# Kernel optimization log

Hardware: AMD Instinct MI355X
Metric: run time of the kernel (lower is better)

## Reference

```python
import jax, jax.numpy as jnp
import numpy as np

N, D, F = 4096, 4096, 16384  # tokens, d_model, d_ff


def setup_inputs() -> dict:
    key = jax.random.key(0)
    ks = jax.random.split(key, 8)
    q_in = jax.random.randint(ks[0], (N, D), -127, 128, dtype=jnp.int32)
    in_scale = jax.random.uniform(ks[1], (N,), dtype=jnp.float32) * 0.01 + 1e-4
    w1_q = jax.random.randint(ks[2], (F, D), -127, 128, dtype=jnp.int32)
    w1_scale = jax.random.uniform(ks[3], (F,), dtype=jnp.float32) * 0.01 + 1e-4
    b1 = jax.random.normal(ks[4], (F,), dtype=jnp.float32) * 0.02
    w2_q = jax.random.randint(ks[5], (D, F), -127, 128, dtype=jnp.int32)
    w2_scale = jax.random.uniform(ks[6], (D,), dtype=jnp.float32) * 0.01 + 1e-4
    b2 = jax.random.normal(ks[7], (D,), dtype=jnp.float32) * 0.02
    return {"q_in": q_in, "in_scale": in_scale, "w1_q": w1_q, "w1_scale": w1_scale,
            "b1": b1, "w2_q": w2_q, "w2_scale": w2_scale, "b2": b2}


def _dynamic_quant(x):
    # per-token abs-max dynamic quantization to int8 range
    s = jnp.max(jnp.abs(x), axis=-1, keepdims=True) / 127.0
    s = jnp.maximum(s, 1e-8)
    q = jnp.clip(jnp.round(x / s), -128.0, 127.0)
    return q, s


def reference(q_in, in_scale, w1_q, w1_scale, b1, w2_q, w2_scale, b2):
    y1 = jnp.einsum('nd,fd->nf', q_in.astype(jnp.float32), w1_q.astype(jnp.float32))
    y1 = y1 * in_scale[:, None] * w1_scale[None, :] + b1[None, :]
    # fused gelu + dynamic re-quantization epilogue
    a = jax.nn.gelu(y1, approximate=False)
    q2, s2 = _dynamic_quant(a)
    # fc2
    y2 = jnp.einsum('nf,df->nd', q2, w2_q.astype(jnp.float32))
    y2 = y2 * s2 * w2_scale[None, :] + b2[None, :]
    return y2
```

## Files before the change

kernel.cpp:

```cpp
#include <hip/hip_runtime.h>
#include <hip/hip_bf16.h>
#include <cstdint>
#include <math.h>

#define TOKENS 4096
#define DMODEL 4096
#define DFF    16384

typedef __attribute__((ext_vector_type(4))) int i32x4;
typedef __attribute__((address_space(1))) unsigned int glb_u32;
typedef __attribute__((address_space(3))) unsigned int lds_u32;

__global__ void pack_i8_kernel(const int* __restrict__ src, unsigned* __restrict__ dst, long n4) {
    long i = (long)blockIdx.x * blockDim.x + threadIdx.x;
    const long stride = (long)gridDim.x * blockDim.x;
    for (; i < n4; i += stride) {
        const int4 v = ((const int4*)src)[i];
        unsigned p = (unsigned(v.x) & 255u) | ((unsigned(v.y) & 255u) << 8) |
                     ((unsigned(v.z) & 255u) << 16) | ((unsigned(v.w) & 255u) << 24);
        dst[i] = p;
    }
}

__global__ void zero_u32_kernel(unsigned* __restrict__ p, int n) {
    int i = blockIdx.x * blockDim.x + threadIdx.x;
    if (i < n) p[i] = 0u;
}

template <int EPI>
__global__ __launch_bounds__(512)
void gemm_i8_kernel(const int8_t* __restrict__ A,
                    const int8_t* __restrict__ B,
                    const int Nout, const int K,
                    const float* __restrict__ scaleA,
                    const float* __restrict__ scaleB,
                    const float* __restrict__ bias,
                    unsigned* __restrict__ rowmax,
                    __hip_bfloat16* __restrict__ aout,
                    float* __restrict__ out)
{
    __shared__ int8_t As[2][256 * 128];
    __shared__ int8_t Bs[2][256 * 128];

    const int tid  = threadIdx.x;
    const int lane = tid & 63;
    const int w    = tid >> 6;
    const int wm   = w >> 2;
    const int wn   = w & 3;
    const int l15  = lane & 15, l4 = lane >> 4;

    const int gx  = gridDim.x;
    const int nwg = gx * gridDim.y;
    int wg = blockIdx.y * gx + blockIdx.x;
    wg = (wg & 7) * (nwg >> 3) + (wg >> 3);
    const int col0 = (wg % gx) * 256;
    const int row0 = (wg / gx) * 256;

    const int nt = K >> 7;

    const int rw = (w << 3) + (lane >> 3);
    const int g16 = ((lane & 7) ^ (lane >> 3)) << 4;

    const int rbA = (((wm << 7) + l15) << 7);
    const int rbB = (((wn << 6) + l15) << 7);
    const int c0  = (l4 ^ (l15 & 7)) << 4;

    i32x4 acc[8][4] = {};

#define STAGE_OP(P, p0q, LDSBUF, t)                                                   \
    {                                                                                 \
        const int k0_ = (t) << 7;                                                     \
        const int8_t* src_ = (P) + (size_t)((p0q) + (w << 3) + (lane >> 3)) * K +     \
                             k0_ + g16;                                               \
        int8_t* dst_ = &LDSBUF[(t) & 1][w << 10];                                     \
        _Pragma("unroll")                                                             \
        for (int u_ = 0; u_ < 4; ++u_)                                                \
            __builtin_amdgcn_global_load_lds((glb_u32*)(src_ + (size_t)(u_ * 64) * K),\
                                             (lds_u32*)(dst_ + u_ * 8192), 16, 0, 0); \
    }

    STAGE_OP(A, row0, As, 0);
    STAGE_OP(B, col0, Bs, 0);
    STAGE_OP(A, row0, As, 1);
    STAGE_OP(B, col0, Bs, 1);
    asm volatile("s_waitcnt vmcnt(8)" ::: "memory");
    __builtin_amdgcn_s_barrier();

    for (int t = 0; t < nt; ++t) {
        const int buf = t & 1;
        const int tn = (t + 2 < nt) ? (t + 2) : (nt - 1);
        i32x4 a0[8], b0[4], a1[8], b1[4];

#pragma unroll
        for (int m = 0; m < 8; ++m)
            a0[m] = *(const i32x4*)(&As[buf][rbA + m * 2048 + c0]);
#pragma unroll
        for (int n = 0; n < 4; ++n)
            b0[n] = *(const i32x4*)(&Bs[buf][rbB + n * 2048 + c0]);
        asm volatile("s_waitcnt lgkmcnt(0)" ::: "memory");
        __builtin_amdgcn_sched_barrier(0);
        __builtin_amdgcn_s_setprio(1);
#pragma unroll
        for (int m = 0; m < 4; ++m)
#pragma unroll
            for (int n = 0; n < 4; ++n)
                acc[m][n] = __builtin_amdgcn_mfma_i32_16x16x64_i8(a0[m], b0[n], acc[m][n], 0, 0, 0);
        __builtin_amdgcn_s_setprio(0);
        __builtin_amdgcn_s_barrier();

#pragma unroll
        for (int m = 0; m < 8; ++m)
            a1[m] = *(const i32x4*)(&As[buf][rbA + m * 2048 + (c0 ^ 64)]);
#pragma unroll
        for (int n = 0; n < 4; ++n)
            b1[n] = *(const i32x4*)(&Bs[buf][rbB + n * 2048 + (c0 ^ 64)]);
        __builtin_amdgcn_s_setprio(1);
#pragma unroll
        for (int m = 4; m < 8; ++m)
#pragma unroll
            for (int n = 0; n < 4; ++n)
                acc[m][n] = __builtin_amdgcn_mfma_i32_16x16x64_i8(a0[m], b0[n], acc[m][n], 0, 0, 0);
        __builtin_amdgcn_s_setprio(0);
        asm volatile("s_waitcnt lgkmcnt(0)" ::: "memory");
        __builtin_amdgcn_sched_barrier(0);
        __builtin_amdgcn_s_barrier();

        STAGE_OP(A, row0, As, tn);
        __builtin_amdgcn_s_setprio(1);
#pragma unroll
        for (int m = 0; m < 4; ++m)
#pragma unroll
            for (int n = 0; n < 4; ++n)
                acc[m][n] = __builtin_amdgcn_mfma_i32_16x16x64_i8(a1[m], b1[n], acc[m][n], 0, 0, 0);
        __builtin_amdgcn_s_setprio(0);
        __builtin_amdgcn_s_barrier();

        STAGE_OP(B, col0, Bs, tn);
        __builtin_amdgcn_s_setprio(1);
#pragma unroll
        for (int m = 4; m < 8; ++m)
#pragma unroll
            for (int n = 0; n < 4; ++n)
                acc[m][n] = __builtin_amdgcn_mfma_i32_16x16x64_i8(a1[m], b1[n], acc[m][n], 0, 0, 0);
        __builtin_amdgcn_s_setprio(0);
        asm volatile("s_waitcnt vmcnt(8)" ::: "memory");
        __builtin_amdgcn_s_barrier();
    }
#undef STAGE_OP

    if (EPI == 1) {
#pragma unroll
        for (int m = 0; m < 8; ++m) {
#pragma unroll
            for (int reg = 0; reg < 4; ++reg) {
                const int grow = row0 + (wm << 7) + m * 16 + l4 * 4 + reg;
                const float sa = scaleA[grow];
                float vmax = 0.0f;
#pragma unroll
                for (int n = 0; n < 4; ++n) {
                    const int gcol = col0 + (wn << 6) + n * 16 + l15;
                    const float y = (float)acc[m][n][reg] * sa * scaleB[gcol] + bias[gcol];
                    const float gl = 0.5f * y * (1.0f + erff(y * 0.70710678118654752f));
                    aout[(size_t)grow * DFF + gcol] = __float2bfloat16(gl);
                    vmax = fmaxf(vmax, fabsf(gl));
                }
#pragma unroll
                for (int off = 1; off < 16; off <<= 1)
                    vmax = fmaxf(vmax, __shfl_xor(vmax, off));
                if (l15 == 0) atomicMax(&rowmax[grow], __float_as_uint(vmax));
            }
        }
    } else {
#pragma unroll
        for (int m = 0; m < 8; ++m) {
#pragma unroll
            for (int reg = 0; reg < 4; ++reg) {
                const int grow = row0 + (wm << 7) + m * 16 + l4 * 4 + reg;
                const float s2 = fmaxf(__uint_as_float(rowmax[grow]) * (1.0f / 127.0f), 1e-8f);
#pragma unroll
                for (int n = 0; n < 4; ++n) {
                    const int gcol = col0 + (wn << 6) + n * 16 + l15;
                    out[(size_t)grow * Nout + gcol] =
                        (float)acc[m][n][reg] * s2 * scaleB[gcol] + bias[gcol];
                }
            }
        }
    }
}

__global__ void quant_kernel(const unsigned short* __restrict__ a,
                             const unsigned* __restrict__ rowmax,
                             int8_t* __restrict__ q2)
{
    const size_t nvec = (size_t)TOKENS * DFF / 8;
    size_t i = (size_t)blockIdx.x * blockDim.x + threadIdx.x;
    const size_t stride = (size_t)gridDim.x * blockDim.x;
    for (; i < nvec; i += stride) {
        const size_t e0 = i * 8;
        const int n = (int)(e0 >> 14);
        const float s2 = fmaxf(__uint_as_float(rowmax[n]) * (1.0f / 127.0f), 1e-8f);
        const float inv = 1.0f / s2;
        const uint4 v = *(const uint4*)(a + e0);
        const unsigned words[4] = {v.x, v.y, v.z, v.w};
        int qi[8];
#pragma unroll
        for (int j = 0; j < 4; ++j) {
            const float f0 = __uint_as_float((words[j] & 0xffffu) << 16);
            const float f1 = __uint_as_float(words[j] & 0xffff0000u);
            qi[2 * j]     = (int)fminf(fmaxf(rintf(f0 * inv), -128.0f), 127.0f);
            qi[2 * j + 1] = (int)fminf(fmaxf(rintf(f1 * inv), -128.0f), 127.0f);
        }
        const unsigned p0 = (unsigned(qi[0]) & 255u) | ((unsigned(qi[1]) & 255u) << 8) |
                            ((unsigned(qi[2]) & 255u) << 16) | ((unsigned(qi[3]) & 255u) << 24);
        const unsigned p1 = (unsigned(qi[4]) & 255u) | ((unsigned(qi[5]) & 255u) << 8) |
                            ((unsigned(qi[6]) & 255u) << 16) | ((unsigned(qi[7]) & 255u) << 24);
        ((uint2*)q2)[i] = make_uint2(p0, p1);
    }
}

extern "C" void kernel_launch(void* const* d_in, const int* in_sizes, int n_in,
                              void* d_out, int out_size, void* d_ws, size_t ws_size,
                              hipStream_t stream) {
    const int*   q_in     = (const int*)d_in[0];
    const float* in_scale = (const float*)d_in[1];
    const int*   w1_q     = (const int*)d_in[2];
    const float* w1_scale = (const float*)d_in[3];
    const float* b1       = (const float*)d_in[4];
    const int*   w2_q     = (const int*)d_in[5];
    const float* w2_scale = (const float*)d_in[6];
    const float* b2       = (const float*)d_in[7];
    float* out = (float*)d_out;

    char* ws = (char*)d_ws;
    int8_t* A1 = (int8_t*)(ws);
    int8_t* W1 = (int8_t*)(ws + (size_t)16  * 1048576);
    int8_t* W2 = (int8_t*)(ws + (size_t)80  * 1048576);
    int8_t* Q2 = (int8_t*)(ws + (size_t)144 * 1048576);
    unsigned short* ABUF = (unsigned short*)(ws + (size_t)208 * 1048576);
    unsigned* ROWMAX = (unsigned*)(ws + (size_t)336 * 1048576);

    zero_u32_kernel<<<dim3(16), dim3(256), 0, stream>>>(ROWMAX, TOKENS);
    pack_i8_kernel<<<dim3(1024), dim3(256), 0, stream>>>(q_in, (unsigned*)A1, (long)TOKENS * DMODEL / 4);
    pack_i8_kernel<<<dim3(4096), dim3(256), 0, stream>>>(w1_q, (unsigned*)W1, (long)DFF * DMODEL / 4);
    pack_i8_kernel<<<dim3(4096), dim3(256), 0, stream>>>(w2_q, (unsigned*)W2, (long)DMODEL * DFF / 4);

    gemm_i8_kernel<1><<<dim3(DFF / 256, TOKENS / 256), dim3(512), 0, stream>>>(
        A1, W1, DFF, DMODEL, in_scale, w1_scale, b1, ROWMAX,
        (__hip_bfloat16*)ABUF, nullptr);

    quant_kernel<<<dim3(4096), dim3(256), 0, stream>>>(ABUF, ROWMAX, Q2);

    gemm_i8_kernel<2><<<dim3(DMODEL / 256, TOKENS / 256), dim3(512), 0, stream>>>(
        Q2, W2, DMODEL, DFF, nullptr, w2_scale, b2, ROWMAX,
        nullptr, out);
}
```

Measured before the change: 851.8 us.

## Switch GEMM to 32x32x32 int8 MFMA with software-pipelined LDS fragment reads

Replaces the 16x16x64 int8 MFMA tiling with 32x32x32 MFMAs, so each wave holds a 4x2 grid of 16-element accumulators, and rewrites the LDS swizzle addressing to match. The K loop now prefetches fragment slices for the next tile before the current tile's last MFMA slice, with graded lgkmcnt waits, to overlap LDS reads with MFMA work. Both global loads for the tile two ahead are issued together after a single barrier. The epilogue row/column mapping and the row-max shuffle reduction are updated for the 32-wide layout. This adds register pressure and depends on the new swizzle mapping being correct.

```diff
diff --git a/kernel.cpp b/kernel.cpp
--- a/kernel.cpp
+++ b/kernel.cpp
@@ -7,7 +7,8 @@
 #define DMODEL 4096
 #define DFF    16384
 
-typedef __attribute__((ext_vector_type(4))) int i32x4;
+typedef __attribute__((ext_vector_type(4)))  int i32x4;
+typedef __attribute__((ext_vector_type(16))) int i32x16;
 typedef __attribute__((address_space(1))) unsigned int glb_u32;
 typedef __attribute__((address_space(3))) unsigned int lds_u32;
 
@@ -47,7 +48,7 @@
     const int w    = tid >> 6;
     const int wm   = w >> 2;
     const int wn   = w & 3;
-    const int l15  = lane & 15, l4 = lane >> 4;
+    const int l31  = lane & 31, l5 = lane >> 5, cx = lane & 7;
 
     const int gx  = gridDim.x;
     const int nwg = gx * gridDim.y;
@@ -58,14 +59,37 @@
 
     const int nt = K >> 7;
 
-    const int rw = (w << 3) + (lane >> 3);
     const int g16 = ((lane & 7) ^ (lane >> 3)) << 4;
 
-    const int rbA = (((wm << 7) + l15) << 7);
-    const int rbB = (((wn << 6) + l15) << 7);
-    const int c0  = (l4 ^ (l15 & 7)) << 4;
-
-    i32x4 acc[8][4] = {};
+    const int rbA = ((wm << 7) + l31) << 7;
+    const int rbB = ((wn << 6) + l31) << 7;
+#define AOFF(m, s) (rbA + (m) * 4096 + (((((s) << 1) | l5) ^ cx) << 4))
+#define BOFF(n, s) (rbB + (n) * 4096 + (((((s) << 1) | l5) ^ cx) << 4))
+
+    i32x4 fA[4][4], fB[4][2];
+    i32x16 acc[4][2] = {};
+
+#define READ_SLICE(s, bufi)                                                       \
+    {                                                                             \
+        _Pragma("unroll")                                                         \
+        for (int m_ = 0; m_ < 4; ++m_)                                            \
+            fA[s][m_] = *(const i32x4*)(&As[bufi][AOFF(m_, s)]);                  \
+        _Pragma("unroll")                                                         \
+        for (int n_ = 0; n_ < 2; ++n_)                                            \
+            fB[s][n_] = *(const i32x4*)(&Bs[bufi][BOFF(n_, s)]);                  \
+    }
+
+#define MFMA_SLICE(s)                                                             \
+    {                                                                             \
+        __builtin_amdgcn_s_setprio(1);                                            \
+        _Pragma("unroll")                                                         \
+        for (int m_ = 0; m_ < 4; ++m_)                                            \
+            _Pragma("unroll")                                                     \
+            for (int n_ = 0; n_ < 2; ++n_)                                        \
+                acc[m_][n_] = __builtin_amdgcn_mfma_i32_32x32x32_i8(              \
+                    fA[s][m_], fB[s][n_], acc[m_][n_], 0, 0, 0);                  \
+        __builtin_amdgcn_s_setprio(0);                                            \
+    }
 
 #define STAGE_OP(P, p0q, LDSBUF, t)                                                   \
     {                                                                                 \
@@ -85,101 +109,80 @@
     STAGE_OP(B, col0, Bs, 1);
     asm volatile("s_waitcnt vmcnt(8)" ::: "memory");
     __builtin_amdgcn_s_barrier();
+    READ_SLICE(0, 0);
+    READ_SLICE(1, 0);
 
     for (int t = 0; t < nt; ++t) {
         const int buf = t & 1;
-        const int tn = (t + 2 < nt) ? (t + 2) : (nt - 1);
-        i32x4 a0[8], b0[4], a1[8], b1[4];
-
-#pragma unroll
-        for (int m = 0; m < 8; ++m)
-            a0[m] = *(const i32x4*)(&As[buf][rbA + m * 2048 + c0]);
-#pragma unroll
-        for (int n = 0; n < 4; ++n)
-            b0[n] = *(const i32x4*)(&Bs[buf][rbB + n * 2048 + c0]);
+        const int tn1 = (t + 1 < nt) ? (t + 1) : (nt - 1);
+        const int tn2 = (t + 2 < nt) ? (t + 2) : (nt - 1);
+
+        READ_SLICE(2, buf);
+        asm volatile("s_waitcnt lgkmcnt(12)" ::: "memory");
+        __builtin_amdgcn_sched_barrier(0);
+        MFMA_SLICE(0);
+
+        READ_SLICE(3, buf);
+        asm volatile("s_waitcnt lgkmcnt(12)" ::: "memory");
+        __builtin_amdgcn_sched_barrier(0);
+        MFMA_SLICE(1);
+
+        asm volatile("s_waitcnt lgkmcnt(6)" ::: "memory");
+        __builtin_amdgcn_sched_barrier(0);
+        MFMA_SLICE(2);
+
         asm volatile("s_waitcnt lgkmcnt(0)" ::: "memory");
         __builtin_amdgcn_sched_barrier(0);
-        __builtin_amdgcn_s_setprio(1);
-#pragma unroll
-        for (int m = 0; m < 4; ++m)
-#pragma unroll
-            for (int n = 0; n < 4; ++n)
-                acc[m][n] = __builtin_amdgcn_mfma_i32_16x16x64_i8(a0[m], b0[n], acc[m][n], 0, 0, 0);
-        __builtin_amdgcn_s_setprio(0);
         __builtin_amdgcn_s_barrier();
 
-#pragma unroll
-        for (int m = 0; m < 8; ++m)
-            a1[m] = *(const i32x4*)(&As[buf][rbA + m * 2048 + (c0 ^ 64)]);
-#pragma unroll
-        for (int n = 0; n < 4; ++n)
-            b1[n] = *(const i32x4*)(&Bs[buf][rbB + n * 2048 + (c0 ^ 64)]);
-        __builtin_amdgcn_s_setprio(1);
-#pragma unroll
-        for (int m = 4; m < 8; ++m)
-#pragma unroll
-            for (int n = 0; n < 4; ++n)
-                acc[m][n] = __builtin_amdgcn_mfma_i32_16x16x64_i8(a0[m], b0[n], acc[m][n], 0, 0, 0);
-        __builtin_amdgcn_s_setprio(0);
-        asm volatile("s_waitcnt lgkmcnt(0)" ::: "memory");
-        __builtin_amdgcn_sched_barrier(0);
-        __builtin_amdgcn_s_barrier();
-
-        STAGE_OP(A, row0, As, tn);
-        __builtin_amdgcn_s_setprio(1);
-#pragma unroll
-        for (int m = 0; m < 4; ++m)
-#pragma unroll
-            for (int n = 0; n < 4; ++n)
-                acc[m][n] = __builtin_amdgcn_mfma_i32_16x16x64_i8(a1[m], b1[n], acc[m][n], 0, 0, 0);
-        __builtin_amdgcn_s_setprio(0);
-        __builtin_amdgcn_s_barrier();
-
-        STAGE_OP(B, col0, Bs, tn);
-        __builtin_amdgcn_s_setprio(1);
-#pragma unroll
-        for (int m = 4; m < 8; ++m)
-#pragma unroll
-            for (int n = 0; n < 4; ++n)
-                acc[m][n] = __builtin_amdgcn_mfma_i32_16x16x64_i8(a1[m], b1[n], acc[m][n], 0, 0, 0);
-        __builtin_amdgcn_s_setprio(0);
+        STAGE_OP(A, row0, As, tn2);
+        STAGE_OP(B, col0, Bs, tn2);
         asm volatile("s_waitcnt vmcnt(8)" ::: "memory");
         __builtin_amdgcn_s_barrier();
+
+        READ_SLICE(0, tn1 & 1);
+        READ_SLICE(1, tn1 & 1);
+        MFMA_SLICE(3);
     }
 #undef STAGE_OP
+#undef READ_SLICE
+#undef MFMA_SLICE
+#undef AOFF
+#undef BOFF
 
     if (EPI == 1) {
 #pragma unroll
-        for (int m = 0; m < 8; ++m) {
-#pragma unroll
-            for (int reg = 0; reg < 4; ++reg) {
-                const int grow = row0 + (wm << 7) + m * 16 + l4 * 4 + reg;
+        for (int m = 0; m < 4; ++m) {
+#pragma unroll
+            for (int reg = 0; reg < 16; ++reg) {
+                const int grow = row0 + (wm << 7) + m * 32 + (reg & 3) + 8 * (reg >> 2) + 4 * l5;
                 const float sa = scaleA[grow];
                 float vmax = 0.0f;
-#pragma unroll
-                for (int n = 0; n < 4; ++n) {
-                    const int gcol = col0 + (wn << 6) + n * 16 + l15;
+                float gl[2];
+#pragma unroll
+                for (int n = 0; n < 2; ++n) {
+                    const int gcol = col0 + (wn << 6) + n * 32 + l31;
                     const float y = (float)acc[m][n][reg] * sa * scaleB[gcol] + bias[gcol];
-                    const float gl = 0.5f * y * (1.0f + erff(y * 0.70710678118654752f));
-                    aout[(size_t)grow * DFF + gcol] = __float2bfloat16(gl);
-                    vmax = fmaxf(vmax, fabsf(gl));
+                    gl[n] = 0.5f * y * (1.0f + erff(y * 0.70710678118654752f));
+                    aout[(size_t)grow * DFF + gcol] = __float2bfloat16(gl[n]);
+                    vmax = fmaxf(vmax, fabsf(gl[n]));
                 }
 #pragma unroll
-                for (int off = 1; off < 16; off <<= 1)
+                for (int off = 1; off < 32; off <<= 1)
                     vmax = fmaxf(vmax, __shfl_xor(vmax, off));
-                if (l15 == 0) atomicMax(&rowmax[grow], __float_as_uint(vmax));
+                if (l31 == 0) atomicMax(&rowmax[grow], __float_as_uint(vmax));
             }
         }
     } else {
 #pragma unroll
-        for (int m = 0; m < 8; ++m) {
-#pragma unroll
-            for (int reg = 0; reg < 4; ++reg) {
-                const int grow = row0 + (wm << 7) + m * 16 + l4 * 4 + reg;
+        for (int m = 0; m < 4; ++m) {
+#pragma unroll
+            for (int reg = 0; reg < 16; ++reg) {
+                const int grow = row0 + (wm << 7) + m * 32 + (reg & 3) + 8 * (reg >> 2) + 4 * l5;
                 const float s2 = fmaxf(__uint_as_float(rowmax[grow]) * (1.0f / 127.0f), 1e-8f);
 #pragma unroll
-                for (int n = 0; n < 4; ++n) {
-                    const int gcol = col0 + (wn << 6) + n * 16 + l15;
+                for (int n = 0; n < 2; ++n) {
+                    const int gcol = col0 + (wn << 6) + n * 32 + l31;
                     out[(size_t)grow * Nout + gcol] =
                         (float)acc[m][n][reg] * s2 * scaleB[gcol] + bias[gcol];
                 }
```

Result: slower. 1.041 ms (+22.3%).

## Restructure int8 GEMM main loop into 1-ahead prefetch with interleaved per-unit loads

Applied to the files above, without the earlier changes.

Replaces the 2-tile-ahead prefetch with a one-tile-ahead double buffer. Global-to-LDS loads are split into per-unit issues placed between the four MFMA quarters, and the A fragments are loaded as half-sized lo/hi groups to cut register use. The aim is to spread memory traffic evenly across the compute phases and lower VGPR pressure. The cost is a shallower prefetch distance, which may expose more global-memory latency, plus extra barriers per iteration.

```diff
diff --git a/kernel.cpp b/kernel.cpp
--- a/kernel.cpp
+++ b/kernel.cpp
@@ -58,95 +58,105 @@
 
     const int nt = K >> 7;
 
-    const int rw = (w << 3) + (lane >> 3);
     const int g16 = ((lane & 7) ^ (lane >> 3)) << 4;
 
     const int rbA = (((wm << 7) + l15) << 7);
     const int rbB = (((wn << 6) + l15) << 7);
     const int c0  = (l4 ^ (l15 & 7)) << 4;
 
+    i32x4 fAlo[4], fAhi[4], fB[4];
     i32x4 acc[8][4] = {};
 
-#define STAGE_OP(P, p0q, LDSBUF, t)                                                   \
+#define STAGE_UNIT(P, p0q, LDSARR, bufi, t, u)                                        \
     {                                                                                 \
-        const int k0_ = (t) << 7;                                                     \
-        const int8_t* src_ = (P) + (size_t)((p0q) + (w << 3) + (lane >> 3)) * K +     \
-                             k0_ + g16;                                               \
-        int8_t* dst_ = &LDSBUF[(t) & 1][w << 10];                                     \
+        const int8_t* src_ = (P) + (size_t)((p0q) + (u) * 64 + (w << 3) +             \
+                             (lane >> 3)) * K + ((t) << 7) + g16;                     \
+        int8_t* dst_ = &LDSARR[bufi][(u) * 8192 + (w << 10)];                         \
+        __builtin_amdgcn_global_load_lds((glb_u32*)src_, (lds_u32*)dst_, 16, 0, 0);   \
+    }
+
+#define MFMA_Q(FA, MB)                                                                \
+    {                                                                                 \
+        __builtin_amdgcn_s_setprio(1);                                                \
         _Pragma("unroll")                                                             \
-        for (int u_ = 0; u_ < 4; ++u_)                                                \
-            __builtin_amdgcn_global_load_lds((glb_u32*)(src_ + (size_t)(u_ * 64) * K),\
-                                             (lds_u32*)(dst_ + u_ * 8192), 16, 0, 0); \
-    }
-
-    STAGE_OP(A, row0, As, 0);
-    STAGE_OP(B, col0, Bs, 0);
-    STAGE_OP(A, row0, As, 1);
-    STAGE_OP(B, col0, Bs, 1);
-    asm volatile("s_waitcnt vmcnt(8)" ::: "memory");
+        for (int m_ = 0; m_ < 4; ++m_)                                                \
+            _Pragma("unroll")                                                         \
+            for (int n_ = 0; n_ < 4; ++n_)                                            \
+                acc[(MB) + m_][n_] = __builtin_amdgcn_mfma_i32_16x16x64_i8(           \
+                    FA[m_], fB[n_], acc[(MB) + m_][n_], 0, 0, 0);                     \
+        __builtin_amdgcn_s_setprio(0);                                                \
+    }
+
+#pragma unroll
+    for (int u = 0; u < 4; ++u) STAGE_UNIT(B, col0, Bs, 0, 0, u);
+#pragma unroll
+    for (int u = 0; u < 4; ++u) STAGE_UNIT(A, row0, As, 0, 0, u);
+    asm volatile("s_waitcnt vmcnt(0)" ::: "memory");
     __builtin_amdgcn_s_barrier();
 
     for (int t = 0; t < nt; ++t) {
-        const int buf = t & 1;
-        const int tn = (t + 2 < nt) ? (t + 2) : (nt - 1);
-        i32x4 a0[8], b0[4], a1[8], b1[4];
-
-#pragma unroll
-        for (int m = 0; m < 8; ++m)
-            a0[m] = *(const i32x4*)(&As[buf][rbA + m * 2048 + c0]);
+        const int buf  = t & 1;
+        const int nbuf = buf ^ 1;
+        const int tn   = (t + 1 < nt) ? (t + 1) : (nt - 1);
+
+#pragma unroll
+        for (int m = 0; m < 4; ++m)
+            fAlo[m] = *(const i32x4*)(&As[buf][rbA + m * 2048 + c0]);
 #pragma unroll
         for (int n = 0; n < 4; ++n)
-            b0[n] = *(const i32x4*)(&Bs[buf][rbB + n * 2048 + c0]);
-        asm volatile("s_waitcnt lgkmcnt(0)" ::: "memory");
-        __builtin_amdgcn_sched_barrier(0);
-        __builtin_amdgcn_s_setprio(1);
-#pragma unroll
-        for (int m = 0; m < 4; ++m)
-#pragma unroll
-            for (int n = 0; n < 4; ++n)
-                acc[m][n] = __builtin_amdgcn_mfma_i32_16x16x64_i8(a0[m], b0[n], acc[m][n], 0, 0, 0);
-        __builtin_amdgcn_s_setprio(0);
-        __builtin_amdgcn_s_barrier();
-
-#pragma unroll
-        for (int m = 0; m < 8; ++m)
-            a1[m] = *(const i32x4*)(&As[buf][rbA + m * 2048 + (c0 ^ 64)]);
+            fB[n] = *(const i32x4*)(&Bs[buf][rbB + n * 2048 + c0]);
+        STAGE_UNIT(B, col0, Bs, nbuf, tn, 0);
+        STAGE_UNIT(B, col0, Bs, nbuf, tn, 1);
+        __builtin_amdgcn_sched_barrier(0);
+        __builtin_amdgcn_s_barrier();
+        asm volatile("s_waitcnt lgkmcnt(0)" ::: "memory");
+        __builtin_amdgcn_sched_barrier(0);
+        MFMA_Q(fAlo, 0);
+        asm volatile("s_waitcnt vmcnt(2)" ::: "memory");
+        __builtin_amdgcn_s_barrier();
+
+#pragma unroll
+        for (int m = 0; m < 4; ++m)
+            fAhi[m] = *(const i32x4*)(&As[buf][rbA + (m + 4) * 2048 + c0]);
+        STAGE_UNIT(B, col0, Bs, nbuf, tn, 2);
+        STAGE_UNIT(B, col0, Bs, nbuf, tn, 3);
+        __builtin_amdgcn_sched_barrier(0);
+        __builtin_amdgcn_s_barrier();
+        asm volatile("s_waitcnt lgkmcnt(0)" ::: "memory");
+        __builtin_amdgcn_sched_barrier(0);
+        MFMA_Q(fAhi, 4);
+        __builtin_amdgcn_s_barrier();
+
+#pragma unroll
+        for (int m = 0; m < 4; ++m)
+            fAlo[m] = *(const i32x4*)(&As[buf][rbA + m * 2048 + (c0 ^ 64)]);
 #pragma unroll
         for (int n = 0; n < 4; ++n)
-            b1[n] = *(const i32x4*)(&Bs[buf][rbB + n * 2048 + (c0 ^ 64)]);
-        __builtin_amdgcn_s_setprio(1);
-#pragma unroll
-        for (int m = 4; m < 8; ++m)
-#pragma unroll
-            for (int n = 0; n < 4; ++n)
-                acc[m][n] = __builtin_amdgcn_mfma_i32_16x16x64_i8(a0[m], b0[n], acc[m][n], 0, 0, 0);
-        __builtin_amdgcn_s_setprio(0);
-        asm volatile("s_waitcnt lgkmcnt(0)" ::: "memory");
-        __builtin_amdgcn_sched_barrier(0);
-        __builtin_amdgcn_s_barrier();
-
-        STAGE_OP(A, row0, As, tn);
-        __builtin_amdgcn_s_setprio(1);
-#pragma unroll
-        for (int m = 0; m < 4; ++m)
-#pragma unroll
-            for (int n = 0; n < 4; ++n)
-                acc[m][n] = __builtin_amdgcn_mfma_i32_16x16x64_i8(a1[m], b1[n], acc[m][n], 0, 0, 0);
-        __builtin_amdgcn_s_setprio(0);
-        __builtin_amdgcn_s_barrier();
-
-        STAGE_OP(B, col0, Bs, tn);
-        __builtin_amdgcn_s_setprio(1);
-#pragma unroll
-        for (int m = 4; m < 8; ++m)
-#pragma unroll
-            for (int n = 0; n < 4; ++n)
-                acc[m][n] = __builtin_amdgcn_mfma_i32_16x16x64_i8(a1[m], b1[n], acc[m][n], 0, 0, 0);
-        __builtin_amdgcn_s_setprio(0);
-        asm volatile("s_waitcnt vmcnt(8)" ::: "memory");
-        __builtin_amdgcn_s_barrier();
-    }
-#undef STAGE_OP
+            fB[n] = *(const i32x4*)(&Bs[buf][rbB + n * 2048 + (c0 ^ 64)]);
+        STAGE_UNIT(A, row0, As, nbuf, tn, 0);
+        STAGE_UNIT(A, row0, As, nbuf, tn, 2);
+        __builtin_amdgcn_sched_barrier(0);
+        __builtin_amdgcn_s_barrier();
+        asm volatile("s_waitcnt lgkmcnt(0)" ::: "memory");
+        __builtin_amdgcn_sched_barrier(0);
+        MFMA_Q(fAlo, 0);
+        __builtin_amdgcn_s_barrier();
+
+#pragma unroll
+        for (int m = 0; m < 4; ++m)
+            fAhi[m] = *(const i32x4*)(&As[buf][rbA + (m + 4) * 2048 + (c0 ^ 64)]);
+        STAGE_UNIT(A, row0, As, nbuf, tn, 1);
+        STAGE_UNIT(A, row0, As, nbuf, tn, 3);
+        __builtin_amdgcn_sched_barrier(0);
+        __builtin_amdgcn_s_barrier();
+        asm volatile("s_waitcnt lgkmcnt(0)" ::: "memory");
+        __builtin_amdgcn_sched_barrier(0);
+        MFMA_Q(fAhi, 4);
+        asm volatile("s_waitcnt vmcnt(2)" ::: "memory");
+        __builtin_amdgcn_s_barrier();
+    }
+#undef STAGE_UNIT
+#undef MFMA_Q
 
     if (EPI == 1) {
 #pragma unroll
```

After: 965.3 us. 13.3% more time.
